# Optimization experiments

Hardware: AMD Instinct MI355X
Metric: run time of the kernel (lower is better)

Reference implementation:

```python
import jax, jax.numpy as jnp
import numpy as np

D_MODEL = 1024
NUM_HEADS = 16
HEAD_DIM = D_MODEL // NUM_HEADS


def setup_inputs() -> dict:
    key = jax.random.key(0)
    ks = jax.random.split(key, 5)
    B, S, D_IN = 2, 2048, 1024
    x = jax.random.normal(ks[0], (B, S, D_IN), dtype=jnp.float32)
    std = 0.02
    wq = jax.random.normal(ks[1], (D_MODEL, D_IN), dtype=jnp.float32) * std
    wk = jax.random.normal(ks[2], (D_MODEL, D_IN), dtype=jnp.float32) * std
    wv = jax.random.normal(ks[3], (D_MODEL, D_IN), dtype=jnp.float32) * std
    wo = jax.random.normal(ks[4], (D_IN, D_MODEL), dtype=jnp.float32) * std
    return {"x": x, "wq": wq, "wk": wk, "wv": wv, "wo": wo}


def _mha(x, wq, wk, wv, wo):
    B, S, _ = x.shape
    H, Dh = NUM_HEADS, HEAD_DIM
    # projections: Linear applies x @ W.T with W of shape [out, in]
    q = (x @ wq.T).reshape(B, S, H, Dh).transpose(0, 2, 1, 3)  # [B,H,S,Dh]
    k = (x @ wk.T).reshape(B, S, H, Dh).transpose(0, 2, 1, 3)
    v = (x @ wv.T).reshape(B, S, H, Dh).transpose(0, 2, 1, 3)
    scores = jnp.einsum('bhqd,bhkd->bhqk', q, k) / jnp.sqrt(jnp.float32(Dh))
    causal = jnp.tril(jnp.ones((S, S), dtype=bool))  # True where attended
    scores = jnp.where(causal, scores, -jnp.inf)
    attn = jax.nn.softmax(scores, axis=-1)
    out = jnp.einsum('bhqk,bhkd->bhqd', attn, v)  # [B,H,S,Dh]
    out = out.transpose(0, 2, 1, 3).reshape(B, S, H * Dh)
    return out @ wo.T


def reference(x, wq, wk, wv, wo):
    return _mha(x, wq, wk, wv, wo)
```

## Files before the change

kernel.cpp:

```cpp
#include <hip/hip_runtime.h>
#include <hip/hip_bf16.h>
#include <stdint.h>

using bf16 = __hip_bfloat16;
typedef __attribute__((ext_vector_type(4))) short shorts4;
typedef __attribute__((ext_vector_type(8))) short short8;
typedef __attribute__((ext_vector_type(4))) float floatx4;
typedef __attribute__((ext_vector_type(16))) float floatx16;
typedef __attribute__((ext_vector_type(4))) unsigned int uintx4;

constexpr int BATCH = 2;
constexpr int SEQ   = 2048;
constexpr int NH    = 16;
constexpr int DH    = 64;
constexpr int DM    = 1024;
constexpr int MROWS = BATCH * SEQ;
constexpr int OUTN  = MROWS * DM;
constexpr int WN    = DM * DM;

__device__ inline short bfbits(float x) {
    bf16 h = __float2bfloat16(x);
    return __builtin_bit_cast(short, h);
}

__device__ inline unsigned pack2(float a, float b) {
    return (unsigned)(unsigned short)bfbits(a) |
           ((unsigned)(unsigned short)bfbits(b) << 16);
}

__device__ inline void async16(bf16* lds, const bf16* g) {
    __builtin_amdgcn_global_load_lds(
        (const __attribute__((address_space(1))) unsigned int*)g,
        (__attribute__((address_space(3))) unsigned int*)lds, 16, 0, 0);
}

__device__ inline void cvt8(const float* src, bf16* dst) {
    float4 f0 = *(const float4*)(src);
    float4 f1 = *(const float4*)(src + 4);
    short8 o;
    o[0] = bfbits(f0.x); o[1] = bfbits(f0.y); o[2] = bfbits(f0.z); o[3] = bfbits(f0.w);
    o[4] = bfbits(f1.x); o[5] = bfbits(f1.y); o[6] = bfbits(f1.z); o[7] = bfbits(f1.w);
    *(short8*)(dst) = o;
}

__global__ __launch_bounds__(256)
void cvt_all(const float* __restrict__ x,  const float* __restrict__ wq,
             const float* __restrict__ wk, const float* __restrict__ wv,
             const float* __restrict__ wo, bf16* __restrict__ dst,
             bf16* __restrict__ wob)
{
    const size_t i = ((size_t)blockIdx.x * 256 + threadIdx.x) * 8;
    if (i < (size_t)OUTN + 3 * WN) {
        const float* src; size_t off;
        if (i < (size_t)OUTN)               { src = x;  off = i; }
        else if (i < (size_t)OUTN + WN)     { src = wq; off = i - OUTN; }
        else if (i < (size_t)OUTN + 2 * WN) { src = wk; off = i - OUTN - WN; }
        else                                { src = wv; off = i - OUTN - 2 * (size_t)WN; }
        cvt8(src + off, dst + i);
    } else {
        const size_t off = i - OUTN - 3 * (size_t)WN;
        cvt8(wo + off, wob + off);
    }
}

__global__ __launch_bounds__(256)
void cvt_inputs(const float* __restrict__ x,  const float* __restrict__ wq,
                const float* __restrict__ wk, const float* __restrict__ wv,
                bf16* __restrict__ dst)
{
    const size_t i = ((size_t)blockIdx.x * 256 + threadIdx.x) * 8;
    const float* src; size_t off;
    if (i < (size_t)OUTN)               { src = x;  off = i; }
    else if (i < (size_t)OUTN + WN)     { src = wq; off = i - OUTN; }
    else if (i < (size_t)OUTN + 2 * WN) { src = wk; off = i - OUTN - WN; }
    else                                { src = wv; off = i - OUTN - 2 * (size_t)WN; }
    cvt8(src + off, dst + i);
}

__global__ __launch_bounds__(256)
void cvt_wo(const float* __restrict__ wo, bf16* __restrict__ dst)
{
    const size_t i = ((size_t)blockIdx.x * 256 + threadIdx.x) * 8;
    cvt8(wo + i, dst + i);
}

template<int MODE, int NT>
__global__ __launch_bounds__(256)
void gemm_mfma(const bf16* __restrict__ A,
               const bf16* __restrict__ W0, const bf16* __restrict__ W1,
               const bf16* __restrict__ W2,
               bf16* __restrict__ C0, bf16* __restrict__ C1, bf16* __restrict__ C2,
               float* __restrict__ F)
{
    constexpr int NJ = NT / 32;
    __shared__ __align__(16) bf16 As[128 * 32];
    __shared__ __align__(16) bf16 Ws[NT * 32];

    const int t    = threadIdx.x;
    const int wave = t >> 6;
    const int lane = t & 63;
    const int quad = lane >> 4;
    const int l16  = lane & 15;
    const int m0 = blockIdx.y * 128;
    const int n0 = blockIdx.x * NT;
    const int wr = (wave >> 1) * 64;
    const int wc = (wave & 1) * (NT / 2);

    const int z = (MODE == 0) ? blockIdx.z : 0;
    const bf16* W = (z == 0) ? W0 : ((z == 1) ? W1 : W2);

    const int c    = t;
    bf16* lA0 = As + c * 8;          bf16* lA1 = As + c * 8 + 2048;
    bf16* lW0 = Ws + c * 8;          bf16* lW1 = Ws + c * 8 + 2048;
    const int ar0 = m0 + (c >> 2),  ar1 = m0 + 64 + (c >> 2);
    const int nr0 = n0 + (c >> 2),  nr1 = n0 + 64 + (c >> 2);
    const int kc  = (c & 3) * 8;

    floatx4 acc[4][NJ] = {};

    for (int k0 = 0; k0 < DM; k0 += 32) {
        const bf16* gA0 = A + (size_t)ar0 * DM + k0 + kc;
        const bf16* gA1 = A + (size_t)ar1 * DM + k0 + kc;
        const bf16* gW0 = W + (size_t)nr0 * DM + k0 + kc;
        const bf16* gW1 = W + (size_t)nr1 * DM + k0 + kc;

        __syncthreads();
        async16(lA0, gA0);
        async16(lA1, gA1);
        async16(lW0, gW0);
        if (NT == 128) async16(lW1, gW1);
        __syncthreads();

        short8 af[4], wf[NJ];
        #pragma unroll
        for (int i = 0; i < 4; i++)
            af[i] = *(const short8*)(As + (wr + i * 16 + l16) * 32 + quad * 8);
        #pragma unroll
        for (int j = 0; j < NJ; j++)
            wf[j] = *(const short8*)(Ws + (wc + j * 16 + l16) * 32 + quad * 8);
        #pragma unroll
        for (int i = 0; i < 4; i++)
            #pragma unroll
            for (int j = 0; j < NJ; j++)
                acc[i][j] = __builtin_amdgcn_mfma_f32_16x16x32_bf16(af[i], wf[j], acc[i][j], 0, 0, 0);
    }

    #pragma unroll
    for (int i = 0; i < 4; i++) {
        #pragma unroll
        for (int j = 0; j < NJ; j++) {
            if (MODE == 0 && z == 2) {
                const int s0 = m0 + wr + i * 16 + quad * 4;
                const int gn = n0 + wc + j * 16 + l16;
                const int b = s0 >> 11, sr = s0 & (SEQ - 1);
                const int h = gn >> 6,  d = gn & (DH - 1);
                shorts4 pv;
                #pragma unroll
                for (int r = 0; r < 4; r++) pv[r] = bfbits(acc[i][j][r]);
                *(shorts4*)(C2 + (((size_t)(b * NH + h)) * DH + d) * SEQ + sr) = pv;
            } else {
                #pragma unroll
                for (int r = 0; r < 4; r++) {
                    const int gm = m0 + wr + i * 16 + quad * 4 + r;
                    const int gn = n0 + wc + j * 16 + l16;
                    if (MODE == 1) {
                        F[(size_t)gm * DM + gn] = acc[i][j][r];
                    } else {
                        float av = acc[i][j][r];
                        if (z == 0) av *= 0.18033688f;
                        bf16* dst = (z == 0) ? C0 : C1;
                        dst[(size_t)gm * DM + gn] = __float2bfloat16(av);
                    }
                }
            }
        }
    }
}

__global__ __launch_bounds__(512, 4)
void attn_flash(bf16* __restrict__ Q, const bf16* __restrict__ K,
                const bf16* __restrict__ Vt)
{
    __shared__ __align__(16) bf16 smem[32768];

    const int t    = threadIdx.x;
    const int wave = t >> 6;
    const int lane = t & 63;
    const int hi   = lane >> 5;
    const int l32  = lane & 31;

    const int h  = blockIdx.y;
    const int b  = blockIdx.z;
    const int qt = (blockIdx.x + 5 * h + 8 * b) & 15;
    const int q0 = qt * 128;
    const int hc = h * DH;
    const size_t rowb = (size_t)b * SEQ;
    const size_t bhv  = ((size_t)(b * NH + h)) * SEQ * DH;

    const int qw    = wave & 3;
    const int khalf = wave >> 2;
    const int qrow  = q0 + qw * 32;
    const int qg    = qrow + l32;

    short8 qf[4];
    #pragma unroll
    for (int s = 0; s < 4; s++)
        qf[s] = *(const short8*)(Q + (rowb + qg) * DM + hc + s * 16 + hi * 8);

    floatx16 oacc[2] = {};
    float lsum = 0.f;

    const int T = q0 / 128 + 1;

    auto stage = [&](int tt, int bb) {
        bf16* Kb = smem + bb * 16384;
        bf16* Vb = Kb + 8192;
        const int k0 = tt * 128;
        #pragma unroll
        for (int p = 0; p < 2; p++) {
            const int ck = p * 512 + t;
            const int kr = ck >> 3;
            const int kg = (ck & 7) ^ (kr & 7);
            async16(Kb + ck * 8, K + (rowb + k0 + kr) * DM + hc + kg * 8);
            const int vr = ck >> 4;
            const int vg = (ck & 15) ^ (vr & 15);
            async16(Vb + ck * 8, Vt + bhv + (size_t)vr * SEQ + k0 + vg * 8);
        }
    };

    stage(0, 0);
    __syncthreads();

    for (int tt = 0; tt < T; ++tt) {
        const int cur = tt & 1;
        if (tt + 1 < T) stage(tt + 1, cur ^ 1);

        const bf16* Ks = smem + cur * 16384;
        const bf16* Vs = Ks + 8192;
        const int kbase = tt * 128 + khalf * 64;

        if (kbase <= qrow + 31) {
            #pragma unroll
            for (int kt = 0; kt < 2; kt++) {
                const int kb = kbase + kt * 32;
                if (kb > qrow + 31) continue;

                const int krow = khalf * 64 + kt * 32 + l32;
                floatx16 sc = {};
                #pragma unroll
                for (int s = 0; s < 4; s++) {
                    const int g = (s * 2 + hi) ^ (krow & 7);
                    short8 kf = *(const short8*)(Ks + krow * 64 + g * 8);
                    sc = __builtin_amdgcn_mfma_f32_32x32x16_bf16(kf, qf[s], sc, 0, 0, 0);
                }

                if (kb + 31 > qrow) {
                    #pragma unroll
                    for (int r = 0; r < 16; r++) {
                        const int key = kb + (r & 3) + 8 * (r >> 2) + 4 * hi;
                        sc[r] = (key <= qg) ? sc[r] : -1e30f;
                    }
                }

                #pragma unroll
                for (int r = 0; r < 16; r++) {
                    const float p = __builtin_amdgcn_exp2f(sc[r]);
                    sc[r] = p;
                    lsum += p;
                }

                unsigned d[4][2];
                #pragma unroll
                for (int g = 0; g < 4; g++) {
                    d[g][0] = pack2(sc[4 * g + 0], sc[4 * g + 1]);
                    d[g][1] = pack2(sc[4 * g + 2], sc[4 * g + 3]);
                }

                #pragma unroll
                for (int h16 = 0; h16 < 2; h16++) {
                    const unsigned a0 = d[h16 * 2][0],     a1 = d[h16 * 2][1];
                    const unsigned b0 = d[h16 * 2 + 1][0], b1 = d[h16 * 2 + 1][1];
                    const unsigned mine0 = hi ? b0 : a0, mine1 = hi ? b1 : a1;
                    const unsigned give0 = hi ? a0 : b0, give1 = hi ? a1 : b1;
                    const unsigned r0 = (unsigned)__shfl_xor((int)give0, 32, 64);
                    const unsigned r1 = (unsigned)__shfl_xor((int)give1, 32, 64);
                    uintx4 pw;
                    pw[0] = hi ? r0 : mine0;
                    pw[1] = hi ? r1 : mine1;
                    pw[2] = hi ? mine0 : r0;
                    pw[3] = hi ? mine1 : r1;
                    short8 pb = __builtin_bit_cast(short8, pw);

                    const int Gbase = khalf * 8 + kt * 4 + h16 * 2 + hi;
                    #pragma unroll
                    for (int tile = 0; tile < 2; tile++) {
                        const int vrow = tile * 32 + l32;
                        const int vg = Gbase ^ (vrow & 15);
                        short8 vf = *(const short8*)(Vs + vrow * 128 + vg * 8);
                        oacc[tile] = __builtin_amdgcn_mfma_f32_32x32x16_bf16(vf, pb, oacc[tile], 0, 0, 0);
                    }
                }
            }
        }
        __syncthreads();
    }

    lsum += __shfl_xor(lsum, 32, 64);

    float* dmp = (float*)smem;
    float* lP  = dmp + 4 * 32 * 65;
    if (wave >= 4) {
        const int p = wave - 4;
        #pragma unroll
        for (int tile = 0; tile < 2; tile++)
            #pragma unroll
            for (int r = 0; r < 16; r++) {
                const int d = tile * 32 + (r & 3) + 8 * (r >> 2) + 4 * hi;
                dmp[(p * 32 + l32) * 65 + d] = oacc[tile][r];
            }
        if (!hi) lP[p * 32 + l32] = lsum;
    }
    __syncthreads();

    if (wave < 4) {
        const int p = wave;
        lsum += lP[p * 32 + l32];
        const float invl = 1.0f / lsum;

        bf16* T8 = smem + 16896 + wave * (32 * 72);
        #pragma unroll
        for (int tile = 0; tile < 2; tile++)
            #pragma unroll
            for (int rq = 0; rq < 4; rq++) {
                shorts4 v4;
                #pragma unroll
                for (int s = 0; s < 4; s++) {
                    const int r = rq * 4 + s;
                    const int d = tile * 32 + (r & 3) + 8 * (r >> 2) + 4 * hi;
                    const float comb = oacc[tile][r] + dmp[(p * 32 + l32) * 65 + d];
                    v4[s] = bfbits(comb * invl);
                }
                *(shorts4*)(T8 + l32 * 72 + tile * 32 + rq * 8 + hi * 4) = v4;
            }
        asm volatile("s_waitcnt lgkmcnt(0)" ::: "memory");
        #pragma unroll
        for (int p2 = 0; p2 < 4; p2++) {
            const int rq = (lane >> 3) + p2 * 8;
            const int dd = (lane & 7) * 8;
            short8 v8 = *(const short8*)(T8 + rq * 72 + dd);
            *(short8*)(Q + (rowb + qrow + rq) * DM + hc + dd) = v8;
        }
    }
}

extern "C" void kernel_launch(void* const* d_in, const int* in_sizes, int n_in,
                              void* d_out, int out_size, void* d_ws, size_t ws_size,
                              hipStream_t stream)
{
    const float* x  = (const float*)d_in[0];
    const float* wq = (const float*)d_in[1];
    const float* wk = (const float*)d_in[2];
    const float* wv = (const float*)d_in[3];
    const float* wo = (const float*)d_in[4];
    float* out = (float*)d_out;

    bf16* qb = (bf16*)d_ws;
    bf16* kb = qb + (size_t)OUTN;
    bf16* vb = kb + (size_t)OUTN;

    bf16* xb  = (bf16*)d_out;
    bf16* wqb = xb + (size_t)OUTN;
    bf16* wkb = wqb + WN;
    bf16* wvb = wkb + WN;

    const bool wsBig = ws_size >= (size_t)(3 * (size_t)OUTN + WN) * sizeof(bf16);

    if (wsBig) {
        bf16* wob = vb + (size_t)OUTN;
        cvt_all<<<(OUTN + 4 * WN) / (8 * 256), 256, 0, stream>>>(
            x, wq, wk, wv, wo, xb, wob);
        gemm_mfma<0, 128><<<dim3(DM / 128, MROWS / 128, 3), dim3(256), 0, stream>>>(
            xb, wqb, wkb, wvb, qb, kb, vb, nullptr);
        attn_flash<<<dim3(SEQ / 128, NH, BATCH), dim3(512), 0, stream>>>(qb, kb, vb);
        gemm_mfma<1, 64><<<dim3(DM / 64, MROWS / 128, 1), dim3(256), 0, stream>>>(
            qb, wob, nullptr, nullptr, nullptr, nullptr, nullptr, out);
    } else {
        cvt_inputs<<<(OUTN + 3 * WN) / (8 * 256), 256, 0, stream>>>(x, wq, wk, wv, xb);
        gemm_mfma<0, 128><<<dim3(DM / 128, MROWS / 128, 3), dim3(256), 0, stream>>>(
            xb, wqb, wkb, wvb, qb, kb, vb, nullptr);
        attn_flash<<<dim3(SEQ / 128, NH, BATCH), dim3(512), 0, stream>>>(qb, kb, vb);
        bf16* wob = kb;
        cvt_wo<<<WN / (8 * 256), 256, 0, stream>>>(wo, wob);
        gemm_mfma<1, 64><<<dim3(DM / 64, MROWS / 128, 1), dim3(256), 0, stream>>>(
            qb, wob, nullptr, nullptr, nullptr, nullptr, nullptr, out);
    }
}
```

Measured before the change: 173.3 us.

## Double-buffer GEMM K-tiles with XOR-swizzled LDS and wider K step

Rewrites the projection GEMM main loop to use two LDS buffers with a K-tile of 64, so the next tile's async loads are issued while MFMAs run on the current one, cutting the loop to one barrier per tile. LDS rows are XOR-swizzled to avoid bank conflicts on the fragment reads, and s_setprio is raised around the MFMA block. The output projection now uses the same 128x128 tile, which halves its grid (256 blocks). The cost is 64KB of LDS per block, which lowers occupancy.

```diff
diff --git a/kernel.cpp b/kernel.cpp
--- a/kernel.cpp
+++ b/kernel.cpp
@@ -92,9 +92,9 @@
                bf16* __restrict__ C0, bf16* __restrict__ C1, bf16* __restrict__ C2,
                float* __restrict__ F)
 {
-    constexpr int NJ = NT / 32;
-    __shared__ __align__(16) bf16 As[128 * 32];
-    __shared__ __align__(16) bf16 Ws[NT * 32];
+    static_assert(NT == 128, "tile fixed at 128x128");
+    constexpr int NJ = 4;
+    __shared__ __align__(16) bf16 smem[32768];
 
     const int t    = threadIdx.x;
     const int wave = t >> 6;
@@ -104,45 +104,59 @@
     const int m0 = blockIdx.y * 128;
     const int n0 = blockIdx.x * NT;
     const int wr = (wave >> 1) * 64;
-    const int wc = (wave & 1) * (NT / 2);
+    const int wc = (wave & 1) * 64;
 
     const int z = (MODE == 0) ? blockIdx.z : 0;
     const bf16* W = (z == 0) ? W0 : ((z == 1) ? W1 : W2);
 
-    const int c    = t;
-    bf16* lA0 = As + c * 8;          bf16* lA1 = As + c * 8 + 2048;
-    bf16* lW0 = Ws + c * 8;          bf16* lW1 = Ws + c * 8 + 2048;
-    const int ar0 = m0 + (c >> 2),  ar1 = m0 + 64 + (c >> 2);
-    const int nr0 = n0 + (c >> 2),  nr1 = n0 + 64 + (c >> 2);
-    const int kc  = (c & 3) * 8;
-
     floatx4 acc[4][NJ] = {};
 
-    for (int k0 = 0; k0 < DM; k0 += 32) {
-        const bf16* gA0 = A + (size_t)ar0 * DM + k0 + kc;
-        const bf16* gA1 = A + (size_t)ar1 * DM + k0 + kc;
-        const bf16* gW0 = W + (size_t)nr0 * DM + k0 + kc;
-        const bf16* gW1 = W + (size_t)nr1 * DM + k0 + kc;
-
+    auto stage = [&](int kt, int bb) {
+        bf16* Ab = smem + bb * 16384;
+        bf16* Wb = Ab + 8192;
+        const int k0 = kt * 64;
+        #pragma unroll
+        for (int p = 0; p < 4; p++) {
+            const int ck = p * 256 + t;
+            const int kr = ck >> 3;
+            const int kg = (ck & 7) ^ (kr & 7);
+            async16(Ab + ck * 8, A + (size_t)(m0 + kr) * DM + k0 + kg * 8);
+            async16(Wb + ck * 8, W + (size_t)(n0 + kr) * DM + k0 + kg * 8);
+        }
+    };
+
+    stage(0, 0);
+    __syncthreads();
+
+    for (int kt = 0; kt < DM / 64; ++kt) {
+        const int cur = kt & 1;
+        if (kt + 1 < DM / 64) stage(kt + 1, cur ^ 1);
+
+        const bf16* Ab = smem + cur * 16384;
+        const bf16* Wb = Ab + 8192;
+
+        #pragma unroll
+        for (int ks = 0; ks < 2; ks++) {
+            short8 af[4], wf[NJ];
+            #pragma unroll
+            for (int i = 0; i < 4; i++) {
+                const int r = wr + i * 16 + l16;
+                af[i] = *(const short8*)(Ab + r * 64 + ((ks * 4 + quad) ^ (r & 7)) * 8);
+            }
+            #pragma unroll
+            for (int j = 0; j < NJ; j++) {
+                const int n = wc + j * 16 + l16;
+                wf[j] = *(const short8*)(Wb + n * 64 + ((ks * 4 + quad) ^ (n & 7)) * 8);
+            }
+            __builtin_amdgcn_s_setprio(1);
+            #pragma unroll
+            for (int i = 0; i < 4; i++)
+                #pragma unroll
+                for (int j = 0; j < NJ; j++)
+                    acc[i][j] = __builtin_amdgcn_mfma_f32_16x16x32_bf16(af[i], wf[j], acc[i][j], 0, 0, 0);
+            __builtin_amdgcn_s_setprio(0);
+        }
         __syncthreads();
-        async16(lA0, gA0);
-        async16(lA1, gA1);
-        async16(lW0, gW0);
-        if (NT == 128) async16(lW1, gW1);
-        __syncthreads();
-
-        short8 af[4], wf[NJ];
-        #pragma unroll
-        for (int i = 0; i < 4; i++)
-            af[i] = *(const short8*)(As + (wr + i * 16 + l16) * 32 + quad * 8);
-        #pragma unroll
-        for (int j = 0; j < NJ; j++)
-            wf[j] = *(const short8*)(Ws + (wc + j * 16 + l16) * 32 + quad * 8);
-        #pragma unroll
-        for (int i = 0; i < 4; i++)
-            #pragma unroll
-            for (int j = 0; j < NJ; j++)
-                acc[i][j] = __builtin_amdgcn_mfma_f32_16x16x32_bf16(af[i], wf[j], acc[i][j], 0, 0, 0);
     }
 
     #pragma unroll
@@ -382,7 +396,7 @@
         gemm_mfma<0, 128><<<dim3(DM / 128, MROWS / 128, 3), dim3(256), 0, stream>>>(
             xb, wqb, wkb, wvb, qb, kb, vb, nullptr);
         attn_flash<<<dim3(SEQ / 128, NH, BATCH), dim3(512), 0, stream>>>(qb, kb, vb);
-        gemm_mfma<1, 64><<<dim3(DM / 64, MROWS / 128, 1), dim3(256), 0, stream>>>(
+        gemm_mfma<1, 128><<<dim3(DM / 128, MROWS / 128, 1), dim3(256), 0, stream>>>(
             qb, wob, nullptr, nullptr, nullptr, nullptr, nullptr, out);
     } else {
         cvt_inputs<<<(OUTN + 3 * WN) / (8 * 256), 256, 0, stream>>>(x, wq, wk, wv, xb);
@@ -391,7 +405,7 @@
         attn_flash<<<dim3(SEQ / 128, NH, BATCH), dim3(512), 0, stream>>>(qb, kb, vb);
         bf16* wob = kb;
         cvt_wo<<<WN / (8 * 256), 256, 0, stream>>>(wo, wob);
-        gemm_mfma<1, 64><<<dim3(DM / 64, MROWS / 128, 1), dim3(256), 0, stream>>>(
+        gemm_mfma<1, 128><<<dim3(DM / 128, MROWS / 128, 1), dim3(256), 0, stream>>>(
             qb, wob, nullptr, nullptr, nullptr, nullptr, nullptr, out);
     }
 }
```

Result: faster. 169.5 us (-2.2%).
